# Optimization experiments

Hardware: AMD Instinct MI355X
Metric: run time of the kernel (lower is better)

Reference implementation:

```python
import jax, jax.numpy as jnp
import numpy as np

B, H, C = 131072, 16, 32        # batch, n_holidays, n_changepoints
HID, HP, SKU = 512, 512 // 16, 64  # hidden_dim, hidden per holiday, sku embed dim
TEMP = 0.7
TIME_MAX = 365.0
LN_EPS = 1e-3  # keras LayerNormalization default epsilon


def mish(x):
    return x * jnp.tanh(jax.nn.softplus(x))


def setup_inputs() -> dict:
    key = jax.random.key(0)
    ks = jax.random.split(key, 12)
    inputs = jax.random.uniform(ks[0], (B, H), dtype=jnp.float32) * TIME_MAX
    sku_embedding = jax.random.normal(ks[1], (B, SKU), dtype=jnp.float32)
    # per-holiday params, stacked over holiday axis
    deltas = jnp.full((H, C), TIME_MAX / C, dtype=jnp.float32)  # changepoint_deltas init
    ln_gamma = jnp.ones((H, C), dtype=jnp.float32)
    ln_beta = jnp.zeros((H, C), dtype=jnp.float32)
    attn_w = jax.random.normal(ks[2], (H,), dtype=jnp.float32) * 0.5  # Dense(1) on [...,1]
    Wh = jax.random.normal(ks[3], (H, C, HP), dtype=jnp.float32) * (1.0 / np.sqrt(C))
    Wah = jax.random.normal(ks[4], (HID, HID), dtype=jnp.float32) * (1.0 / np.sqrt(HID))
    Waa = jax.random.normal(ks[5], (HID, HID), dtype=jnp.float32) * (1.0 / np.sqrt(HID))
    Wb = jax.random.normal(ks[6], (SKU, HID), dtype=jnp.float32) * (1.0 / np.sqrt(SKU))
    Wa = jax.random.normal(ks[7], (SKU, HID), dtype=jnp.float32) * (1.0 / np.sqrt(SKU))
    Wo = jax.random.normal(ks[8], (HID, 1), dtype=jnp.float32)
    Wo = Wo / jnp.linalg.norm(Wo, axis=0, keepdims=True)  # UnitNorm(axis=0) constraint
    return {"inputs": inputs, "sku_embedding": sku_embedding, "deltas": deltas,
            "ln_gamma": ln_gamma, "ln_beta": ln_beta, "attn_w": attn_w, "Wh": Wh,
            "Wah": Wah, "Waa": Waa, "Wb": Wb, "Wa": Wa, "Wo": Wo}


def reference(inputs, sku_embedding, deltas, ln_gamma, ln_beta, attn_w, Wh, Wah, Waa, Wb, Wa, Wo):
    # ChangepointReLU (vectorised over holidays): softplus -> cumsum -> rescale to [0, 365]
    pd = jax.nn.softplus(deltas)                     # [H, C]
    cps = jnp.cumsum(pd, axis=-1)
    cps = cps / cps[:, -1:] * TIME_MAX               # time_min = 0
    feats = jax.nn.relu(inputs[:, :, None] - cps[None, :, :])  # [B, H, C]
    # per-holiday LayerNorm over changepoint axis
    mu = jnp.mean(feats, axis=-1, keepdims=True)
    var = jnp.mean((feats - mu) ** 2, axis=-1, keepdims=True)
    normed = (feats - mu) * jax.lax.rsqrt(var + LN_EPS) * ln_gamma[None] + ln_beta[None]
    # per-holiday attention: Dense(1,no bias) on [...,1] == scalar multiply per holiday
    logits = normed * attn_w[None, :, None]
    attn = jax.nn.softmax(logits / TEMP, axis=-1)    # n_changepoints > 1
    attended = normed * attn                          # [B, H, C]
    # per-holiday hidden Dense(HP, mish, no bias), then concat over holidays
    hid = mish(jnp.einsum('bhc,hcd->bhd', attended, Wh))  # [B, H, HP]
    aggregated = hid.reshape(hid.shape[0], H * HP)        # [B, HID]
    agg_hidden = mish(aggregated @ Wah)                   # [B, HID]
    agg_attn = jax.nn.softmax((agg_hidden @ Waa) / TEMP, axis=-1)
    final = agg_hidden * agg_attn                         # dropout inactive (inference)
    beta = jax.nn.sigmoid(sku_embedding @ Wb)
    alpha = sku_embedding @ Wa
    final = final * beta + alpha
    return final @ Wo                                     # [B, 1]
```

## Files before the change

### kernel.cpp

```cpp
#include <hip/hip_runtime.h>
#include <hip/hip_fp16.h>
#include <stdint.h>

#define B_TOT 131072
#define CHUNK 65536
#define NH 16
#define NC 32
#define HIDD 512

typedef unsigned short u16;
typedef unsigned int u32;
typedef __attribute__((ext_vector_type(8))) short short8;
typedef __attribute__((ext_vector_type(4))) float f32x4;
typedef __attribute__((ext_vector_type(4))) int i32x4;

#define GLLDS(g, l) __builtin_amdgcn_global_load_lds((const __attribute__((address_space(1))) unsigned int*)(g), (__attribute__((address_space(3))) unsigned int*)(l), 16, 0, 0)

__device__ __forceinline__ u16 f2bf(float x){
  unsigned u = __float_as_uint(x);
  u += 0x7fffu + ((u >> 16) & 1u);
  return (u16)(u >> 16);
}
__device__ __forceinline__ float bf2f(u16 b){ return __uint_as_float(((unsigned)b) << 16); }
__device__ __forceinline__ u16 f2h(float x){ __half h = __float2half(x); return *(u16*)&h; }
__device__ __forceinline__ float h2f(u16 b){ __half h; *(u16*)&h = b; return __half2float(h); }
__device__ __forceinline__ float mishf(float x){
  float e = __expf(fminf(x, 30.f));
  float u = 1.f + e;
  float u2 = u * u;
  return x * (u2 - 1.f) / (u2 + 1.f);
}

__global__ void prep_small(const float* __restrict__ deltas, const float* __restrict__ Wa,
                           const float* __restrict__ Wo, float* __restrict__ cps, float* __restrict__ wWo)
{
  const int t = threadIdx.x;
  if (t < NH){
    float cum[NC];
    float run = 0.f;
#pragma unroll
    for (int c = 0; c < NC; c++){
      float d = deltas[t*NC + c];
      float sp = (d > 20.f) ? d : log1pf(__expf(d));
      run += sp; cum[c] = run;
    }
    float s = 365.0f / run;
#pragma unroll
    for (int c = 0; c < NC; c++) cps[t*NC + c] = cum[c] * s;
  } else if (t >= 64 && t < 128){
    const int k = t - 64;
    float s = 0.f;
    for (int n = 0; n < HIDD; n++) s += Wa[k*HIDD + n] * Wo[n];
    wWo[k] = s;
  }
}

__global__ void prep_convert(const float* __restrict__ Wah, const float* __restrict__ Waa,
                             const float* __restrict__ Wb, const float* __restrict__ Wh,
                             u16* __restrict__ WahT, u16* __restrict__ WaaT,
                             u16* __restrict__ WbT, u16* __restrict__ WhT)
{
  int i = blockIdx.x * 256 + threadIdx.x;
  if (i < 262144){ int n = i >> 9, k = i & 511; WahT[i] = f2bf(Wah[k*512 + n]); return; }
  i -= 262144;
  if (i < 262144){ int n = i >> 9, k = i & 511; WaaT[i] = f2bf(Waa[k*512 + n]); return; }
  i -= 262144;
  if (i < 32768){ int n = i >> 6, k = i & 63; WbT[i] = f2bf(Wb[k*512 + n]); return; }
  i -= 32768;
  if (i < 16384){ int h = i >> 10, r = i & 1023, d = r >> 5, c = r & 31;
                  WhT[i] = f2bf(Wh[h*1024 + c*32 + d]); return; }
}

__global__ __launch_bounds__(256) void stage1_kernel(
    const float* __restrict__ inputs, const float* __restrict__ sku,
    const float* __restrict__ ln_g, const float* __restrict__ ln_b,
    const float* __restrict__ attnw, const float* __restrict__ cps,
    const float* __restrict__ wWo, const u16* __restrict__ WhT,
    u16* __restrict__ agg, u16* __restrict__ skub, float* __restrict__ skd)
{
  __shared__ __align__(16) float in_l[256];
  __shared__ __align__(16) float cps_l[512];
  __shared__ __align__(16) float gam_l[512];
  __shared__ __align__(16) float bet_l[512];
  __shared__ float aw_l[16];
  __shared__ __align__(16) u16 at_l[16*16*32];
  __shared__ __align__(16) u16 ot_l[16*512];

  const int t = threadIdx.x;
  const int ln = t & 63;
  const long bb = (long)blockIdx.x * 16;

  in_l[t] = inputs[bb*16 + t];
  cps_l[t] = cps[t];       cps_l[t+256] = cps[t+256];
  gam_l[t] = ln_g[t];      gam_l[t+256] = ln_g[t+256];
  bet_l[t] = ln_b[t];      bet_l[t+256] = ln_b[t+256];
  if (t < 16) aw_l[t] = attnw[t];
  {
    const f32x4 sv = *(const f32x4*)&sku[bb*64 + t*4];
    unsigned lo = (unsigned)f2bf(sv.x) | ((unsigned)f2bf(sv.y) << 16);
    unsigned hi = (unsigned)f2bf(sv.z) | ((unsigned)f2bf(sv.w) << 16);
    unsigned long long v = (unsigned long long)lo | ((unsigned long long)hi << 32);
    *(unsigned long long*)&skub[bb*64 + t*4] = v;
    const f32x4 wv4 = *(const f32x4*)&wWo[(ln & 15)*4];
    float pd = sv.x*wv4.x + sv.y*wv4.y + sv.z*wv4.z + sv.w*wv4.w;
#pragma unroll
    for (int s = 1; s < 16; s <<= 1) pd += __shfl_xor(pd, s);
    if ((ln & 15) == 0) skd[bb + (t >> 4)] = pd;
  }
  __syncthreads();

  const int h = t >> 4, bi = t & 15;
  const float x = in_l[bi*16 + h];
  float nrm[NC], pw[NC];
  float s1 = 0.f;
#pragma unroll
  for (int c = 0; c < NC; c++){ float f = fmaxf(x - cps_l[h*NC + c], 0.f); nrm[c] = f; s1 += f; }
  const float mu = s1 * (1.f/NC);
  float s2 = 0.f;
#pragma unroll
  for (int c = 0; c < NC; c++){ float d = nrm[c] - mu; s2 += d*d; }
  const float rs = rsqrtf(s2 * (1.f/NC) + 1e-3f);
  const float aw = aw_l[h] * (1.0f/0.7f);
  float lmax = -1e30f;
#pragma unroll
  for (int c = 0; c < NC; c++){
    float nv = (nrm[c] - mu) * rs * gam_l[h*NC + c] + bet_l[h*NC + c];
    nrm[c] = nv;
    lmax = fmaxf(lmax, nv * aw);
  }
  float ps = 0.f;
#pragma unroll
  for (int c = 0; c < NC; c++){ float p = __expf(nrm[c]*aw - lmax); pw[c] = p; ps += p; }
  const float invs = 1.f / ps;
#pragma unroll
  for (int c = 0; c < NC; c += 2){
    unsigned pk = (unsigned)f2bf(nrm[c]*pw[c]*invs) | ((unsigned)f2bf(nrm[c+1]*pw[c+1]*invs) << 16);
    *(unsigned*)&at_l[h*512 + bi*32 + c] = pk;
  }
  __syncthreads();

  const int wv = t >> 6;
  const int lrow = ln & 15, lq = ln >> 4;
#pragma unroll
  for (int q = 0; q < 4; q++){
    const int hh = wv*4 + q;
    short8 af  = *(const short8*)&at_l[hh*512 + lrow*32 + lq*8];
    short8 bf0 = *(const short8*)&WhT[hh*1024 + lrow*32 + lq*8];
    short8 bf1 = *(const short8*)&WhT[hh*1024 + (16 + lrow)*32 + lq*8];
    f32x4 acc0 = {0.f,0.f,0.f,0.f}, acc1 = {0.f,0.f,0.f,0.f};
    acc0 = __builtin_amdgcn_mfma_f32_16x16x32_bf16(af, bf0, acc0, 0, 0, 0);
    acc1 = __builtin_amdgcn_mfma_f32_16x16x32_bf16(af, bf1, acc1, 0, 0, 0);
#pragma unroll
    for (int r = 0; r < 4; r++){
      const int br = lq*4 + r;
      ot_l[br*512 + hh*32 + lrow]      = f2bf(mishf(acc0[r]));
      ot_l[br*512 + hh*32 + 16 + lrow] = f2bf(mishf(acc1[r]));
    }
  }
  __syncthreads();
  {
    const int row = t >> 4, c16 = t & 15;
    const i32x4* src = (const i32x4*)&ot_l[row*512 + c16*32];
    i32x4* dst = (i32x4*)&agg[(bb + row)*512 + c16*32];
#pragma unroll
    for (int j = 0; j < 4; j++) dst[j] = src[j];
  }
}

__global__ __launch_bounds__(256, 3) void gemm_bw(
    const u16* __restrict__ A, const u16* __restrict__ Bt,
    const float* __restrict__ Wo, u16* __restrict__ bw)
{
  __shared__ __align__(16) u16 As[2][128*32];
  __shared__ __align__(16) u16 Bs[2][128*32];
  const int t = threadIdx.x, wv = t >> 6, ln = t & 63;
  const int g = blockIdx.x;
  const int m_idx = (g & 7) + ((g >> 5) << 3);
  const int n_idx = (g >> 3) & 3;
  const long m0 = (long)m_idx * 128;
  const int n0 = n_idx * 128;
  const int lrow = ln & 15, lq = ln >> 4;
  const int wm = wv >> 1, wn = wv & 1;

  auto stage = [&](int buf, int kt){
#pragma unroll
    for (int p = 0; p < 2; p++){
      const int chunk = p*256 + wv*64 + ln;
      const int mm = chunk >> 2, kc = chunk & 3;
      const int kcl = kc ^ ((mm >> 1) & 3);
      GLLDS(&A[(m0 + mm)*64 + kt + kcl*8],  &As[buf][(p*256 + wv*64)*8]);
      GLLDS(&Bt[(n0 + mm)*64 + kt + kcl*8], &Bs[buf][(p*256 + wv*64)*8]);
    }
  };

  f32x4 acc[4][4] = {};
  stage(0, 0);
  for (int ks = 0; ks < 2; ks++){
    const int cur = ks & 1;
    __syncthreads();
    if (ks + 1 < 2) stage(cur ^ 1, (ks + 1)*32);
    short8 a[4], b[4];
#pragma unroll
    for (int i = 0; i < 4; i++){
      const int ra = wm*64 + i*16 + lrow;
      const int rb = wn*64 + i*16 + lrow;
      const int lqa = lq ^ ((ra >> 1) & 3);
      const int lqb = lq ^ ((rb >> 1) & 3);
      a[i] = *(const short8*)&As[cur][ra*32 + lqa*8];
      b[i] = *(const short8*)&Bs[cur][rb*32 + lqb*8];
    }
#pragma unroll
    for (int i = 0; i < 4; i++)
#pragma unroll
      for (int j = 0; j < 4; j++)
        acc[i][j] = __builtin_amdgcn_mfma_f32_16x16x32_bf16(a[i], b[j], acc[i][j], 0, 0, 0);
  }
#pragma unroll
  for (int j = 0; j < 4; j++){
    const int n = n0 + wn*64 + j*16 + lrow;
    const float wo = Wo[n];
#pragma unroll
    for (int i = 0; i < 4; i++){
#pragma unroll
      for (int r = 0; r < 4; r++){
        const long m = m0 + wm*64 + i*16 + lq*4 + r;
        const float sig = 1.f / (1.f + __expf(-acc[i][j][r]));
        bw[m*512 + n] = f2h(sig * wo);
      }
    }
  }
}

__global__ __launch_bounds__(256, 3) void gemm1(
    const u16* __restrict__ A, const u16* __restrict__ Bt, u16* __restrict__ aggh)
{
  __shared__ __align__(16) u16 smem[24576];
  const int t = threadIdx.x, wv = t >> 6, ln = t & 63;
  const int g = blockIdx.x;
  const int m_idx = (g & 7) + ((g >> 5) << 3);
  const int n_idx = (g >> 3) & 3;
  const long m0 = (long)m_idx * 128;
  const int n0 = n_idx * 128;
  const int lrow = ln & 15, lq = ln >> 4;
  const int wm = wv >> 1, wn = wv & 1;

  auto stage = [&](int buf, int kt){
#pragma unroll
    for (int p = 0; p < 2; p++){
      const int chunk = p*256 + wv*64 + ln;
      const int mm = chunk >> 2, kc = chunk & 3;
      const int kcl = kc ^ ((mm >> 1) & 3);
      GLLDS(&A[(m0 + mm)*512 + kt + kcl*8],  &smem[buf*4096 + (p*256 + wv*64)*8]);
      GLLDS(&Bt[(n0 + mm)*512 + kt + kcl*8], &smem[12288 + buf*4096 + (p*256 + wv*64)*8]);
    }
  };

  f32x4 acc[4][4] = {};
  stage(0, 0); stage(1, 32);
#pragma unroll 1
  for (int ks = 0; ks < 16; ks++){
    const int cur = ks % 3;
    if (ks < 15) asm volatile("s_waitcnt vmcnt(4)" ::: "memory");
    else         asm volatile("s_waitcnt vmcnt(0)" ::: "memory");
    __builtin_amdgcn_s_barrier();
    if (ks + 2 < 16) stage((ks + 2) % 3, (ks + 2)*32);
    short8 a[4], b[4];
#pragma unroll
    for (int i = 0; i < 4; i++){
      const int ra = wm*64 + i*16 + lrow;
      const int rb = wn*64 + i*16 + lrow;
      const int lqa = lq ^ ((ra >> 1) & 3);
      const int lqb = lq ^ ((rb >> 1) & 3);
      a[i] = *(const short8*)&smem[cur*4096 + ra*32 + lqa*8];
      b[i] = *(const short8*)&smem[12288 + cur*4096 + rb*32 + lqb*8];
    }
#pragma unroll
    for (int i = 0; i < 4; i++)
#pragma unroll
      for (int j = 0; j < 4; j++)
        acc[i][j] = __builtin_amdgcn_mfma_f32_16x16x32_bf16(a[i], b[j], acc[i][j], 0, 0, 0);
  }

  const int TP = 136;
  __syncthreads();
#pragma unroll 1
  for (int h = 0; h < 2; h++){
    if (wm == h){
#pragma unroll
      for (int i = 0; i < 4; i++)
#pragma unroll
        for (int j = 0; j < 4; j++)
#pragma unroll
          for (int r = 0; r < 4; r++)
            smem[(i*16 + lq*4 + r)*TP + wn*64 + j*16 + lrow] = f2bf(mishf(acc[i][j][r]));
    }
    __syncthreads();
#pragma unroll
    for (int it = 0; it < 4; it++){
      const int idx = it*256 + t;
      const int row = idx >> 4, ch = idx & 15;
      const i32x4 v = *(const i32x4*)&smem[row*TP + ch*8];
      *(i32x4*)&aggh[(m0 + h*64 + row)*512 + n0 + ch*8] = v;
    }
    __syncthreads();
  }
}

__global__ __launch_bounds__(256, 3) void mega2p(
    const u16* __restrict__ A, const u16* __restrict__ Bt,
    const u16* __restrict__ bw, float* __restrict__ part)
{
  __shared__ __align__(16) u16 smem[24576];
  const int t = threadIdx.x, wv = t >> 6, ln = t & 63;
  const int g = blockIdx.x;
  const int m_idx = (g & 7) + ((g >> 5) << 3);
  const int n_idx = (g >> 3) & 3;
  const long m0 = (long)m_idx * 128;
  const int n0 = n_idx * 128;
  const int lrow = ln & 15, lq = ln >> 4;
  const int wm = wv >> 1, wn = wv & 1;

  auto stage = [&](int buf, int kt){
#pragma unroll
    for (int p = 0; p < 2; p++){
      const int chunk = p*256 + wv*64 + ln;
      const int mm = chunk >> 2, kc = chunk & 3;
      const int kcl = kc ^ ((mm >> 1) & 3);
      GLLDS(&A[(m0 + mm)*512 + kt + kcl*8],  &smem[buf*4096 + (p*256 + wv*64)*8]);
      GLLDS(&Bt[(n0 + mm)*512 + kt + kcl*8], &smem[12288 + buf*4096 + (p*256 + wv*64)*8]);
    }
  };

  f32x4 acc[4][4] = {};
  stage(0, 0); stage(1, 32);
#pragma unroll 1
  for (int ks = 0; ks < 16; ks++){
    const int cur = ks % 3;
    if (ks < 15) asm volatile("s_waitcnt vmcnt(4)" ::: "memory");
    else         asm volatile("s_waitcnt vmcnt(0)" ::: "memory");
    __builtin_amdgcn_s_barrier();
    if (ks + 2 < 16) stage((ks + 2) % 3, (ks + 2)*32);
    short8 a[4], b[4];
#pragma unroll
    for (int i = 0; i < 4; i++){
      const int ra = wm*64 + i*16 + lrow;
      const int rb = wn*64 + i*16 + lrow;
      const int lqa = lq ^ ((ra >> 1) & 3);
      const int lqb = lq ^ ((rb >> 1) & 3);
      a[i] = *(const short8*)&smem[cur*4096 + ra*32 + lqa*8];
      b[i] = *(const short8*)&smem[12288 + cur*4096 + rb*32 + lqb*8];
    }
#pragma unroll
    for (int i = 0; i < 4; i++)
#pragma unroll
      for (int j = 0; j < 4; j++)
        acc[i][j] = __builtin_amdgcn_mfma_f32_16x16x32_bf16(a[i], b[j], acc[i][j], 0, 0, 0);
  }

  __syncthreads();
  float* mloc = (float*)smem;
  float* sloc = mloc + 256;
  float* tloc = sloc + 256;
  const float inv_t = 1.0f / 0.7f;

#pragma unroll
  for (int i = 0; i < 4; i++){
#pragma unroll
    for (int r = 0; r < 4; r++){
      float tm = acc[i][0][r];
#pragma unroll
      for (int j = 1; j < 4; j++) tm = fmaxf(tm, acc[i][j][r]);
#pragma unroll
      for (int s = 1; s < 16; s <<= 1) tm = fmaxf(tm, __shfl_xor(tm, s));
      float sp = 0.f, tp = 0.f;
#pragma unroll
      for (int j = 0; j < 4; j++){
        const long gi = (m0 + wm*64 + i*16 + lq*4 + r)*512 + n0 + wn*64 + j*16 + lrow;
        const float e = __expf((acc[i][j][r] - tm) * inv_t);
        sp += e;
        tp += e * bf2f(A[gi]) * h2f(bw[gi]);
      }
#pragma unroll
      for (int s = 1; s < 16; s <<= 1){ sp += __shfl_xor(sp, s); tp += __shfl_xor(tp, s); }
      if (lrow == 0){
        const int row = wm*64 + i*16 + lq*4 + r;
        mloc[row*2 + wn] = tm; sloc[row*2 + wn] = sp; tloc[row*2 + wn] = tp;
      }
    }
  }
  __syncthreads();
  if (t < 128){
    const float ma = mloc[t*2], mb = mloc[t*2 + 1];
    const float M = fmaxf(ma, mb);
    const float wa = __expf((ma - M) * inv_t), wb = __expf((mb - M) * inv_t);
    const float S = sloc[t*2]*wa + sloc[t*2 + 1]*wb;
    const float T = tloc[t*2]*wa + tloc[t*2 + 1]*wb;
    float* pm = part + (size_t)n_idx*3*CHUNK;
    pm[m0 + t]           = M;
    pm[CHUNK + m0 + t]   = S;
    pm[2*CHUNK + m0 + t] = T;
  }
}

__global__ __launch_bounds__(256) void combine_kernel(
    const float* __restrict__ part, const float* __restrict__ skd, float* __restrict__ outp)
{
  const int row = blockIdx.x*256 + threadIdx.x;
  const float inv_t = 1.0f / 0.7f;
  float M = -1e30f;
#pragma unroll
  for (int nt = 0; nt < 4; nt++) M = fmaxf(M, part[(size_t)nt*3*CHUNK + row]);
  float S = 0.f, T = 0.f;
#pragma unroll
  for (int nt = 0; nt < 4; nt++){
    const float w = __expf((part[(size_t)nt*3*CHUNK + row] - M) * inv_t);
    S += part[(size_t)nt*3*CHUNK + CHUNK + row] * w;
    T += part[(size_t)nt*3*CHUNK + 2*CHUNK + row] * w;
  }
  outp[row] = T / S + skd[row];
}

__global__ void ws_too_small(float* o, float v){ o[(long)blockIdx.x*256 + threadIdx.x] = v; }

extern "C" void kernel_launch(void* const* d_in, const int* in_sizes, int n_in,
                              void* d_out, int out_size, void* d_ws, size_t ws_size,
                              hipStream_t stream)
{
  const float* inputs = (const float*)d_in[0];
  const float* sku    = (const float*)d_in[1];
  const float* deltas = (const float*)d_in[2];
  const float* ln_g   = (const float*)d_in[3];
  const float* ln_b   = (const float*)d_in[4];
  const float* attnw  = (const float*)d_in[5];
  const float* Wh     = (const float*)d_in[6];
  const float* Wah    = (const float*)d_in[7];
  const float* Waa    = (const float*)d_in[8];
  const float* Wb     = (const float*)d_in[9];
  const float* Wa     = (const float*)d_in[10];
  const float* Wo     = (const float*)d_in[11];
  float* outp = (float*)d_out;

  const size_t OFF_CPS  = 0;
  const size_t OFF_WWO  = 2048;
  const size_t OFF_WAHT = 4096;
  const size_t OFF_WAAT = OFF_WAHT + 524288;
  const size_t OFF_WBT  = OFF_WAAT + 524288;
  const size_t OFF_WHT  = OFF_WBT  + 65536;
  const size_t OFF_SKUB = OFF_WHT  + 32768;
  const size_t OFF_SKD  = OFF_SKUB + (size_t)CHUNK*64*2;
  const size_t OFF_AGG  = OFF_SKD  + (size_t)CHUNK*4;
  const size_t OFF_BW   = OFF_AGG  + (size_t)CHUNK*512*2;
  const size_t OFF_AGH  = OFF_BW   + (size_t)CHUNK*512*2;
  const size_t OFF_PART = OFF_AGH  + (size_t)CHUNK*512*2;
  const size_t NEED     = OFF_PART + (size_t)4*3*CHUNK*4;

  if (ws_size < NEED){
    hipLaunchKernelGGL(ws_too_small, dim3(B_TOT/256), dim3(256), 0, stream,
                       outp, -(float)(ws_size >> 20));
    return;
  }

  char* ws = (char*)d_ws;
  float* cps  = (float*)(ws + OFF_CPS);
  float* wWo  = (float*)(ws + OFF_WWO);
  u16* WahT   = (u16*)(ws + OFF_WAHT);
  u16* WaaT   = (u16*)(ws + OFF_WAAT);
  u16* WbT    = (u16*)(ws + OFF_WBT);
  u16* WhT    = (u16*)(ws + OFF_WHT);
  u16* skub   = (u16*)(ws + OFF_SKUB);
  float* skd  = (float*)(ws + OFF_SKD);
  u16* agg    = (u16*)(ws + OFF_AGG);
  u16* bw     = (u16*)(ws + OFF_BW);
  u16* aggh   = (u16*)(ws + OFF_AGH);
  float* part = (float*)(ws + OFF_PART);

  hipLaunchKernelGGL(prep_small, dim3(1), dim3(128), 0, stream, deltas, Wa, Wo, cps, wWo);
  hipLaunchKernelGGL(prep_convert, dim3(2240), dim3(256), 0, stream,
                     Wah, Waa, Wb, Wh, WahT, WaaT, WbT, WhT);

  for (int ch = 0; ch < B_TOT / CHUNK; ch++){
    const float* in_c  = inputs + (size_t)ch * CHUNK * 16;
    const float* sku_c = sku    + (size_t)ch * CHUNK * 64;
    float* out_c       = outp   + (size_t)ch * CHUNK;

    hipLaunchKernelGGL(stage1_kernel, dim3(CHUNK/16), dim3(256), 0, stream,
                       in_c, sku_c, ln_g, ln_b, attnw, cps, wWo, WhT, agg, skub, skd);
    hipLaunchKernelGGL(gemm_bw, dim3(CHUNK/128*4), dim3(256), 0, stream,
                       skub, WbT, Wo, bw);
    hipLaunchKernelGGL(gemm1, dim3(CHUNK/128*4), dim3(256), 0, stream,
                       agg, WahT, aggh);
    hipLaunchKernelGGL(mega2p, dim3(CHUNK/128*4), dim3(256), 0, stream,
                       aggh, WaaT, bw, part);
    hipLaunchKernelGGL(combine_kernel, dim3(CHUNK/256), dim3(256), 0, stream,
                       part, skd, out_c);
  }
}
```

Measured before the change: 520.2 us.

## Fuse sigmoid(sku@Wb)*Wo GEMM into final kernel and stage aggh tile in LDS

Removes the separate gemm_bw kernel and its fp16 bw intermediate buffer. The mega2f kernel now computes the small K=64 sku@Wb GEMM at its start and keeps the sigmoid*Wo values packed in registers. It also stages the aggh tile into LDS with a swizzle, replacing the scattered global reads in the softmax epilogue. Stage1 drops the pw array and recomputes the exps instead, to save registers. This removes a write and a read of a 64MB intermediate per chunk and one launch, at the cost of more register pressure and extra exp work in the fused kernel.

```diff
diff --git a/kernel.cpp b/kernel.cpp
--- a/kernel.cpp
+++ b/kernel.cpp
@@ -111,7 +111,7 @@
 
   const int h = t >> 4, bi = t & 15;
   const float x = in_l[bi*16 + h];
-  float nrm[NC], pw[NC];
+  float nrm[NC];
   float s1 = 0.f;
 #pragma unroll
   for (int c = 0; c < NC; c++){ float f = fmaxf(x - cps_l[h*NC + c], 0.f); nrm[c] = f; s1 += f; }
@@ -130,11 +130,13 @@
   }
   float ps = 0.f;
 #pragma unroll
-  for (int c = 0; c < NC; c++){ float p = __expf(nrm[c]*aw - lmax); pw[c] = p; ps += p; }
+  for (int c = 0; c < NC; c++) ps += __expf(nrm[c]*aw - lmax);
   const float invs = 1.f / ps;
 #pragma unroll
   for (int c = 0; c < NC; c += 2){
-    unsigned pk = (unsigned)f2bf(nrm[c]*pw[c]*invs) | ((unsigned)f2bf(nrm[c+1]*pw[c+1]*invs) << 16);
+    const float p0 = __expf(nrm[c]*aw - lmax) * invs;
+    const float p1 = __expf(nrm[c+1]*aw - lmax) * invs;
+    unsigned pk = (unsigned)f2bf(nrm[c]*p0) | ((unsigned)f2bf(nrm[c+1]*p1) << 16);
     *(unsigned*)&at_l[h*512 + bi*32 + c] = pk;
   }
   __syncthreads();
@@ -164,70 +166,6 @@
     i32x4* dst = (i32x4*)&agg[(bb + row)*512 + c16*32];
 #pragma unroll
     for (int j = 0; j < 4; j++) dst[j] = src[j];
-  }
-}
-
-__global__ __launch_bounds__(256, 3) void gemm_bw(
-    const u16* __restrict__ A, const u16* __restrict__ Bt,
-    const float* __restrict__ Wo, u16* __restrict__ bw)
-{
-  __shared__ __align__(16) u16 As[2][128*32];
-  __shared__ __align__(16) u16 Bs[2][128*32];
-  const int t = threadIdx.x, wv = t >> 6, ln = t & 63;
-  const int g = blockIdx.x;
-  const int m_idx = (g & 7) + ((g >> 5) << 3);
-  const int n_idx = (g >> 3) & 3;
-  const long m0 = (long)m_idx * 128;
-  const int n0 = n_idx * 128;
-  const int lrow = ln & 15, lq = ln >> 4;
-  const int wm = wv >> 1, wn = wv & 1;
-
-  auto stage = [&](int buf, int kt){
-#pragma unroll
-    for (int p = 0; p < 2; p++){
-      const int chunk = p*256 + wv*64 + ln;
-      const int mm = chunk >> 2, kc = chunk & 3;
-      const int kcl = kc ^ ((mm >> 1) & 3);
-      GLLDS(&A[(m0 + mm)*64 + kt + kcl*8],  &As[buf][(p*256 + wv*64)*8]);
-      GLLDS(&Bt[(n0 + mm)*64 + kt + kcl*8], &Bs[buf][(p*256 + wv*64)*8]);
-    }
-  };
-
-  f32x4 acc[4][4] = {};
-  stage(0, 0);
-  for (int ks = 0; ks < 2; ks++){
-    const int cur = ks & 1;
-    __syncthreads();
-    if (ks + 1 < 2) stage(cur ^ 1, (ks + 1)*32);
-    short8 a[4], b[4];
-#pragma unroll
-    for (int i = 0; i < 4; i++){
-      const int ra = wm*64 + i*16 + lrow;
-      const int rb = wn*64 + i*16 + lrow;
-      const int lqa = lq ^ ((ra >> 1) & 3);
-      const int lqb = lq ^ ((rb >> 1) & 3);
-      a[i] = *(const short8*)&As[cur][ra*32 + lqa*8];
-      b[i] = *(const short8*)&Bs[cur][rb*32 + lqb*8];
-    }
-#pragma unroll
-    for (int i = 0; i < 4; i++)
-#pragma unroll
-      for (int j = 0; j < 4; j++)
-        acc[i][j] = __builtin_amdgcn_mfma_f32_16x16x32_bf16(a[i], b[j], acc[i][j], 0, 0, 0);
-  }
-#pragma unroll
-  for (int j = 0; j < 4; j++){
-    const int n = n0 + wn*64 + j*16 + lrow;
-    const float wo = Wo[n];
-#pragma unroll
-    for (int i = 0; i < 4; i++){
-#pragma unroll
-      for (int r = 0; r < 4; r++){
-        const long m = m0 + wm*64 + i*16 + lq*4 + r;
-        const float sig = 1.f / (1.f + __expf(-acc[i][j][r]));
-        bw[m*512 + n] = f2h(sig * wo);
-      }
-    }
   }
 }
 
@@ -306,9 +244,10 @@
   }
 }
 
-__global__ __launch_bounds__(256, 3) void mega2p(
+__global__ __launch_bounds__(256, 3) void mega2f(
     const u16* __restrict__ A, const u16* __restrict__ Bt,
-    const u16* __restrict__ bw, float* __restrict__ part)
+    const u16* __restrict__ skub, const u16* __restrict__ WbT,
+    const float* __restrict__ Wo, float* __restrict__ part)
 {
   __shared__ __align__(16) u16 smem[24576];
   const int t = threadIdx.x, wv = t >> 6, ln = t & 63;
@@ -319,6 +258,56 @@
   const int n0 = n_idx * 128;
   const int lrow = ln & 15, lq = ln >> 4;
   const int wm = wv >> 1, wn = wv & 1;
+  const float inv_t = 1.0f / 0.7f;
+
+  u32 bwp[4][4][2];
+  {
+    auto stage3 = [&](int buf, int kt){
+#pragma unroll
+      for (int p = 0; p < 2; p++){
+        const int chunk = p*256 + wv*64 + ln;
+        const int mm = chunk >> 2, kc = chunk & 3;
+        const int kcl = kc ^ ((mm >> 1) & 3);
+        GLLDS(&skub[(m0 + mm)*64 + kt + kcl*8], &smem[buf*4096 + (p*256 + wv*64)*8]);
+        GLLDS(&WbT[(n0 + mm)*64 + kt + kcl*8],  &smem[8192 + buf*4096 + (p*256 + wv*64)*8]);
+      }
+    };
+    f32x4 acc3[4][4] = {};
+    stage3(0, 0); stage3(1, 32);
+    asm volatile("s_waitcnt vmcnt(0)" ::: "memory");
+    __builtin_amdgcn_s_barrier();
+#pragma unroll
+    for (int ks3 = 0; ks3 < 2; ks3++){
+      short8 a3[4], b3[4];
+#pragma unroll
+      for (int i = 0; i < 4; i++){
+        const int ra = wm*64 + i*16 + lrow;
+        const int rb = wn*64 + i*16 + lrow;
+        const int lqa = lq ^ ((ra >> 1) & 3);
+        const int lqb = lq ^ ((rb >> 1) & 3);
+        a3[i] = *(const short8*)&smem[ks3*4096 + ra*32 + lqa*8];
+        b3[i] = *(const short8*)&smem[8192 + ks3*4096 + rb*32 + lqb*8];
+      }
+#pragma unroll
+      for (int i = 0; i < 4; i++)
+#pragma unroll
+        for (int j = 0; j < 4; j++)
+          acc3[i][j] = __builtin_amdgcn_mfma_f32_16x16x32_bf16(a3[i], b3[j], acc3[i][j], 0, 0, 0);
+    }
+#pragma unroll
+    for (int j = 0; j < 4; j++){
+      const float wo = Wo[n0 + wn*64 + j*16 + lrow];
+#pragma unroll
+      for (int i = 0; i < 4; i++)
+#pragma unroll
+        for (int rp = 0; rp < 2; rp++){
+          const float s0 = wo / (1.f + __expf(-acc3[i][j][2*rp]));
+          const float s1 = wo / (1.f + __expf(-acc3[i][j][2*rp+1]));
+          bwp[i][j][rp] = (u32)f2h(s0) | ((u32)f2h(s1) << 16);
+        }
+    }
+  }
+  __syncthreads();
 
   auto stage = [&](int buf, int kt){
 #pragma unroll
@@ -358,10 +347,18 @@
   }
 
   __syncthreads();
-  float* mloc = (float*)smem;
+#pragma unroll
+  for (int it = 0; it < 8; it++){
+    const int idx = it*256 + wv*64 + ln;
+    const int row = idx >> 4, gcol = idx & 15;
+    GLLDS(&A[(m0 + row)*512 + n0 + ((gcol ^ (row & 7)) << 3)], &smem[(it*256 + wv*64)*8]);
+  }
+  asm volatile("s_waitcnt vmcnt(0)" ::: "memory");
+  __syncthreads();
+
+  float* mloc = (float*)&smem[16384];
   float* sloc = mloc + 256;
   float* tloc = sloc + 256;
-  const float inv_t = 1.0f / 0.7f;
 
 #pragma unroll
   for (int i = 0; i < 4; i++){
@@ -372,19 +369,20 @@
       for (int j = 1; j < 4; j++) tm = fmaxf(tm, acc[i][j][r]);
 #pragma unroll
       for (int s = 1; s < 16; s <<= 1) tm = fmaxf(tm, __shfl_xor(tm, s));
+      const int rowL = wm*64 + i*16 + lq*4 + r;
       float sp = 0.f, tp = 0.f;
 #pragma unroll
       for (int j = 0; j < 4; j++){
-        const long gi = (m0 + wm*64 + i*16 + lq*4 + r)*512 + n0 + wn*64 + j*16 + lrow;
+        const int colL = wn*64 + j*16 + lrow;
         const float e = __expf((acc[i][j][r] - tm) * inv_t);
-        sp += e;
-        tp += e * bf2f(A[gi]) * h2f(bw[gi]);
+        const float av = bf2f(smem[rowL*128 + (((colL >> 3) ^ (rowL & 7)) << 3) + (colL & 7)]);
+        const u16 bh = (u16)(bwp[i][j][r >> 1] >> ((r & 1)*16));
+        sp += e; tp += e * av * h2f(bh);
       }
 #pragma unroll
       for (int s = 1; s < 16; s <<= 1){ sp += __shfl_xor(sp, s); tp += __shfl_xor(tp, s); }
       if (lrow == 0){
-        const int row = wm*64 + i*16 + lq*4 + r;
-        mloc[row*2 + wn] = tm; sloc[row*2 + wn] = sp; tloc[row*2 + wn] = tp;
+        mloc[rowL*2 + wn] = tm; sloc[rowL*2 + wn] = sp; tloc[rowL*2 + wn] = tp;
       }
     }
   }
@@ -449,8 +447,7 @@
   const size_t OFF_SKUB = OFF_WHT  + 32768;
   const size_t OFF_SKD  = OFF_SKUB + (size_t)CHUNK*64*2;
   const size_t OFF_AGG  = OFF_SKD  + (size_t)CHUNK*4;
-  const size_t OFF_BW   = OFF_AGG  + (size_t)CHUNK*512*2;
-  const size_t OFF_AGH  = OFF_BW   + (size_t)CHUNK*512*2;
+  const size_t OFF_AGH  = OFF_AGG  + (size_t)CHUNK*512*2;
   const size_t OFF_PART = OFF_AGH  + (size_t)CHUNK*512*2;
   const size_t NEED     = OFF_PART + (size_t)4*3*CHUNK*4;
 
@@ -470,7 +467,6 @@
   u16* skub   = (u16*)(ws + OFF_SKUB);
   float* skd  = (float*)(ws + OFF_SKD);
   u16* agg    = (u16*)(ws + OFF_AGG);
-  u16* bw     = (u16*)(ws + OFF_BW);
   u16* aggh   = (u16*)(ws + OFF_AGH);
   float* part = (float*)(ws + OFF_PART);
 
@@ -485,12 +481,10 @@
 
     hipLaunchKernelGGL(stage1_kernel, dim3(CHUNK/16), dim3(256), 0, stream,
                        in_c, sku_c, ln_g, ln_b, attnw, cps, wWo, WhT, agg, skub, skd);
-    hipLaunchKernelGGL(gemm_bw, dim3(CHUNK/128*4), dim3(256), 0, stream,
-                       skub, WbT, Wo, bw);
     hipLaunchKernelGGL(gemm1, dim3(CHUNK/128*4), dim3(256), 0, stream,
                        agg, WahT, aggh);
-    hipLaunchKernelGGL(mega2p, dim3(CHUNK/128*4), dim3(256), 0, stream,
-                       aggh, WaaT, bw, part);
+    hipLaunchKernelGGL(mega2f, dim3(CHUNK/128*4), dim3(256), 0, stream,
+                       aggh, WaaT, skub, WbT, Wo, part);
     hipLaunchKernelGGL(combine_kernel, dim3(CHUNK/256), dim3(256), 0, stream,
                        part, skd, out_c);
   }
```

New measurement: 485.4 us. -6.7%, faster.
